# Kernel tuning notes

Measured on AMD Instinct MI355X. Metric: run time of the kernel, lower is better.

The kernel has to match this reference:

```python
import jax, jax.numpy as jnp
import numpy as np

N = 5000        # n_stocks (nodes)
F = 128         # n_features
H = 4           # attention heads
C = 32          # hidden_size per head
HC = H * C      # GAT output dim = GRU input dim
GH = 256        # gru_hidden_size
E = 320000      # directed edges (before self-loops)
NEG_SLOPE = 0.2 # GATv2Conv default leaky_relu slope


def setup_inputs() -> dict:
    key = jax.random.key(0)
    ks = jax.random.split(key, 16)
    s = 0.05
    return {
        "x": jax.random.normal(ks[0], (N, F), dtype=jnp.float32),
        "edge_index": jax.random.randint(ks[1], (2, E), 0, N, dtype=jnp.int64),
        # GATv2Conv params (lin_l, lin_r with bias, attention vector, output bias)
        "W_l": jax.random.normal(ks[2], (F, HC), dtype=jnp.float32) * s,
        "b_l": jax.random.normal(ks[3], (HC,), dtype=jnp.float32) * s,
        "W_r": jax.random.normal(ks[4], (F, HC), dtype=jnp.float32) * s,
        "b_r": jax.random.normal(ks[5], (HC,), dtype=jnp.float32) * s,
        "att": jax.random.normal(ks[6], (H, C), dtype=jnp.float32) * s,
        "gat_bias": jax.random.normal(ks[7], (HC,), dtype=jnp.float32) * s,
        # GRU params (single layer, PyTorch gate order r,z,n)
        "W_ih": jax.random.normal(ks[8], (3 * GH, HC), dtype=jnp.float32) * s,
        "W_hh": jax.random.normal(ks[9], (3 * GH, GH), dtype=jnp.float32) * s,
        "b_ih": jax.random.normal(ks[10], (3 * GH,), dtype=jnp.float32) * s,
        "b_hh": jax.random.normal(ks[11], (3 * GH,), dtype=jnp.float32) * s,
        # policy head + log_std param
        "Wp": jax.random.normal(ks[12], (N, GH), dtype=jnp.float32) * s,
        "bp": jax.random.normal(ks[13], (N,), dtype=jnp.float32) * s,
        "log_std": jnp.zeros((N,), dtype=jnp.float32),
    }


def reference(x, edge_index, W_l, b_l, W_r, b_r, att, gat_bias,
              W_ih, W_hh, b_ih, b_hh, Wp, bp, log_std):
    # --- GATv2Conv (add_self_loops=True, concat heads, eval mode -> no dropout) ---
    loop = jnp.arange(N, dtype=edge_index.dtype)
    src = jnp.concatenate([edge_index[0], loop])  # message source j
    dst = jnp.concatenate([edge_index[1], loop])  # message target i

    xl = (x @ W_l + b_l).reshape(N, H, C)  # source-side transform
    xr = (x @ W_r + b_r).reshape(N, H, C)  # target-side transform

    m = xl[src] + xr[dst]                                  # [Etot, H, C]
    e = jnp.einsum('ehc,hc->eh', jax.nn.leaky_relu(m, NEG_SLOPE), att)

    # segment softmax over incoming edges per target node
    emax = jax.ops.segment_max(e, dst, num_segments=N)      # [N, H]
    ex = jnp.exp(e - emax[dst])
    denom = jax.ops.segment_sum(ex, dst, num_segments=N)    # [N, H]
    alpha = ex / denom[dst]                                 # [Etot, H]

    agg = jax.ops.segment_sum(alpha[:, :, None] * xl[src], dst, num_segments=N)
    gat_out = agg.reshape(N, HC) + gat_bias                 # [N, H*C]

    # --- GRU: each node = one batch element, seq_len=1, h0 = 0 ---
    gi = gat_out @ W_ih.T + b_ih                            # [N, 3*GH]
    gr, gz, gn = jnp.split(gi, 3, axis=1)
    hr, hz, hn = jnp.split(b_hh, 3)                          # h0=0 -> only hh bias
    r = jax.nn.sigmoid(gr + hr)
    z = jax.nn.sigmoid(gz + hz)
    n = jnp.tanh(gn + r * hn)
    h = (1.0 - z) * n                                        # [N, GH]

    # --- policy head ---
    mean = h @ Wp.T + bp                                     # [N, N]
    std = jnp.exp(jnp.clip(log_std, -10.0, 2.0))             # [N]
    return mean, std
```

## Files before the change

### kernel.cpp

```cpp
#include <hip/hip_runtime.h>
#include <hip/hip_bf16.h>
#include <float.h>

#define N_NODES 5000
#define F_IN    128
#define HC      128
#define GH      256
#define NE      320000
#define NET     325000
#define MPAD    5120
#define CAP     160
#define LIN_BLKS   313
#define DEC_BLKS  1270
#define NTHR    (DEC_BLKS * 256)

typedef __bf16 bf16;
typedef __attribute__((ext_vector_type(4))) __bf16 bf16x4;
typedef __attribute__((ext_vector_type(8))) __bf16 bf16x8;
typedef __attribute__((ext_vector_type(4))) float  f32x4;

__device__ __forceinline__ float lrelu(float v) { return v > 0.f ? v : 0.2f * v; }
__device__ __forceinline__ float sigm(float v) { return 1.f / (1.f + __expf(-v)); }

__device__ __forceinline__ void gload16(const void* g, void* l) {
  __builtin_amdgcn_global_load_lds((const __attribute__((address_space(1))) void*)g,
                                   (__attribute__((address_space(3))) void*)l, 16, 0, 0);
}

__global__ void k_init(int* __restrict__ cnt) {
  int i = blockIdx.x * 256 + threadIdx.x;
  if (i < N_NODES) cnt[i] = 0;
}

#define NWIH (768 * HC)
#define NWP  (N_NODES * GH)
__global__ __launch_bounds__(256) void k_pre(
    const float* __restrict__ x,
    const float* __restrict__ Wl, const float* __restrict__ bl,
    const float* __restrict__ Wr, const float* __restrict__ br,
    bf16* __restrict__ xlb, bf16* __restrict__ xrb,
    const float* __restrict__ lstd, float* __restrict__ out_std,
    const int* __restrict__ ei, int* __restrict__ cnt, int* __restrict__ csr_s,
    const float* __restrict__ wih, const float* __restrict__ wp,
    bf16* __restrict__ wihb, bf16* __restrict__ wpb) {
  __shared__ float xs[16][F_IN];
  int t = threadIdx.x;
  if (blockIdx.x < LIN_BLKS) {
    int nb = blockIdx.x * 16;
#pragma unroll
    for (int p = 0; p < 8; ++p) {
      int idx = p * 256 + t;
      int nl = idx >> 7, c = idx & 127;
      int gn = nb + nl;
      xs[nl][c] = (gn < N_NODES) ? x[(size_t)gn * F_IN + c] : 0.f;
    }
    __syncthreads();
    int col = t & 127;
    const float* W = (t < 128) ? Wl : Wr;
    float bias = (t < 128) ? bl[col] : br[col];
    float acc[16];
#pragma unroll
    for (int m = 0; m < 16; ++m) acc[m] = bias;
#pragma unroll 4
    for (int k = 0; k < F_IN; ++k) {
      float w = W[k * HC + col];
#pragma unroll
      for (int m = 0; m < 16; ++m) acc[m] = fmaf(xs[m][k], w, acc[m]);
    }
    bf16* out = (t < 128) ? xlb : xrb;
#pragma unroll
    for (int m = 0; m < 16; ++m) {
      int gn = nb + m;
      if (gn < N_NODES) out[(size_t)gn * HC + col] = (bf16)acc[m];
    }
    if (t < 16) {
      int gn = nb + t;
      if (gn < N_NODES) out_std[gn] = expf(fminf(fmaxf(lstd[gn], -10.f), 2.f));
    }
    return;
  }
  __shared__ int mode;
  if (t == 0) {
    int f = 0;
    for (int q = 1; q < 128; q += 2) f |= ei[q];
    mode = (f == 0) ? 1 : 0;
  }
  __syncthreads();
  int e = (blockIdx.x - LIN_BLKS) * 256 + t;
  for (int i = e; i < NWIH / 4; i += NTHR) {
    float4 v = reinterpret_cast<const float4*>(wih)[i];
    bf16x4 o = {(bf16)v.x, (bf16)v.y, (bf16)v.z, (bf16)v.w};
    *reinterpret_cast<bf16x4*>(&wihb[i * 4]) = o;
  }
  for (int i = e; i < NWP / 4; i += NTHR) {
    float4 v = reinterpret_cast<const float4*>(wp)[i];
    bf16x4 o = {(bf16)v.x, (bf16)v.y, (bf16)v.z, (bf16)v.w};
    *reinterpret_cast<bf16x4*>(&wpb[i * 4]) = o;
  }
  if (e >= NET) return;
  int s, d;
  if (e >= NE) { s = d = e - NE; }
  else if (mode) {
    int2 sv = *reinterpret_cast<const int2*>(&ei[2 * e]);
    int2 dv = *reinterpret_cast<const int2*>(&ei[2 * (NE + e)]);
    s = sv.x; d = dv.x;
  } else { s = ei[e]; d = ei[NE + e]; }
  int slot = atomicAdd(&cnt[d], 1);
  if (slot < CAP) csr_s[d * CAP + slot] = s;
}

__global__ __launch_bounds__(256) void k_gat(
    const bf16* __restrict__ xlb, const bf16* __restrict__ xrb,
    const int* __restrict__ csr_s, const int* __restrict__ cnt,
    const float* __restrict__ att, const float* __restrict__ gbias,
    bf16* __restrict__ gat_b) {
  int t = threadIdx.x;
  int lane = t & 63;
  int node = blockIdx.x * 4 + (t >> 6);
  if (node >= N_NODES) return;
  int c8 = lane & 15;
  int eg = lane >> 4;
  bf16x8 xr8 = *reinterpret_cast<const bf16x8*>(xrb + (size_t)node * HC + c8 * 8);
  float4 w0 = reinterpret_cast<const float4*>(att)[c8 * 2];
  float4 w1 = reinterpret_cast<const float4*>(att)[c8 * 2 + 1];
  float xr[8], wv[8];
#pragma unroll
  for (int k = 0; k < 8; ++k) xr[k] = (float)xr8[k];
  wv[0] = w0.x; wv[1] = w0.y; wv[2] = w0.z; wv[3] = w0.w;
  wv[4] = w1.x; wv[5] = w1.y; wv[6] = w1.z; wv[7] = w1.w;

  float acc[8] = {0.f, 0.f, 0.f, 0.f, 0.f, 0.f, 0.f, 0.f};
  float den = 0.f;
  int deg = cnt[node];
  deg = deg < CAP ? deg : CAP;
  int beg = node * CAP, end = node * CAP + deg;
#pragma unroll 2
  for (int p0 = beg; p0 < end; p0 += 4) {
    int p = p0 + eg;
    bool valid = p < end;
    int j = valid ? csr_s[p] : node;
    bf16x8 a8 = *reinterpret_cast<const bf16x8*>(xlb + (size_t)j * HC + c8 * 8);
    float av[8];
    float tt = 0.f;
#pragma unroll
    for (int k = 0; k < 8; ++k) {
      av[k] = (float)a8[k];
      tt = fmaf(lrelu(av[k] + xr[k]), wv[k], tt);
    }
    tt += __shfl_xor(tt, 1);
    tt += __shfl_xor(tt, 2);
    float pe = valid ? __expf(tt) : 0.f;
    den += pe;
#pragma unroll
    for (int k = 0; k < 8; ++k) acc[k] = fmaf(pe, av[k], acc[k]);
  }
#pragma unroll
  for (int m = 16; m <= 32; m <<= 1) {
    den += __shfl_xor(den, m);
#pragma unroll
    for (int k = 0; k < 8; ++k) acc[k] += __shfl_xor(acc[k], m);
  }
  if (eg == 0) {
    float4 g0 = reinterpret_cast<const float4*>(gbias)[c8 * 2];
    float4 g1 = reinterpret_cast<const float4*>(gbias)[c8 * 2 + 1];
    float gb[8] = {g0.x, g0.y, g0.z, g0.w, g1.x, g1.y, g1.z, g1.w};
    float rden = 1.f / den;
    bf16x8 o;
#pragma unroll
    for (int k = 0; k < 8; ++k) o[k] = (bf16)(acc[k] * rden + gb[k]);
    *reinterpret_cast<bf16x8*>(gat_b + (size_t)node * HC + c8 * 8) = o;
  }
}

__global__ __launch_bounds__(256) void k_gemm_gru(
    const bf16* __restrict__ A, const bf16* __restrict__ wihb,
    const float* __restrict__ bih, const float* __restrict__ bhh,
    bf16* __restrict__ hb) {
  __shared__ char smem[73728];
  char* Ab = smem;
  int t = threadIdx.x;
  int lane = t & 63, wave = t >> 6;
  int wm = wave >> 1, wn = wave & 1;
  int r16 = lane & 15, kg = lane >> 4;
  int sw7 = r16 & 7;
  int bm = blockIdx.x >> 1, bn = blockIdx.x & 1;
  int r0 = bm * 32, c0 = bn * 128;

#pragma unroll
  for (int q = 0; q < 2; ++q) {
    int idx = q * 256 + t;
    int half = idx >> 8, ih = idx & 255;
    int row = ih >> 3, cc = ih & 7;
    int gc = cc ^ (row & 7);
    gload16(&A[(size_t)(r0 + row) * 128 + half * 64 + gc * 8],
            Ab + (q * 256 + wave * 64) * 16);
  }

  auto STAGE_B = [&](int gate, int buf) {
    char* Bb = smem + 8192 + buf * 32768;
#pragma unroll
    for (int q = 0; q < 8; ++q) {
      int idx = q * 256 + t;
      int half = idx >> 10, ih = idx & 1023;
      int row = ih >> 3, cc = ih & 7;
      int gc = cc ^ (row & 7);
      gload16(&wihb[(size_t)(gate * 256 + c0 + row) * 128 + half * 64 + gc * 8],
              Bb + (q * 256 + wave * 64) * 16);
    }
  };

  int rowA = (wm * 16 + r16) * 128;
  int rowB[4];
#pragma unroll
  for (int n = 0; n < 4; ++n) rowB[n] = (wn * 64 + n * 16 + r16) * 128;

  f32x4 acc[3][4] = {};
  STAGE_B(0, 0);
  __syncthreads();
#pragma unroll
  for (int g = 0; g < 3; ++g) {
    if (g < 2) STAGE_B(g + 1, (g + 1) & 1);
    const char* Bb = smem + 8192 + (g & 1) * 32768;
#pragma unroll
    for (int h = 0; h < 2; ++h)
#pragma unroll
      for (int w = 0; w < 2; ++w) {
        int ch = ((w * 4 + kg) ^ sw7) * 16;
        bf16x8 af = *reinterpret_cast<const bf16x8*>(Ab + h * 4096 + rowA + ch);
        bf16x8 bfr[4];
#pragma unroll
        for (int n = 0; n < 4; ++n)
          bfr[n] = *reinterpret_cast<const bf16x8*>(Bb + h * 16384 + rowB[n] + ch);
#pragma unroll
        for (int n = 0; n < 4; ++n)
          acc[g][n] = __builtin_amdgcn_mfma_f32_16x16x32_bf16(af, bfr[n], acc[g][n], 0, 0, 0);
      }
    __syncthreads();
  }

  bf16* hl = (bf16*)Ab;
#pragma unroll
  for (int n = 0; n < 4; ++n) {
    int c = c0 + wn * 64 + n * 16 + r16;
    float bihr = bih[c],       bhhr = bhh[c];
    float bihz = bih[256 + c], bhhz = bhh[256 + c];
    float bihn = bih[512 + c], bhhn = bhh[512 + c];
#pragma unroll
    for (int rr = 0; rr < 4; ++rr) {
      float rg = sigm(acc[0][n][rr] + bihr + bhhr);
      float zg = sigm(acc[1][n][rr] + bihz + bhhz);
      float ng = tanhf(acc[2][n][rr] + bihn + rg * bhhn);
      float hv = (1.f - zg) * ng;
      int row = wm * 16 + kg * 4 + rr;
      hl[row * 128 + (wn * 64 + n * 16 + r16)] = (bf16)hv;
    }
  }
  __syncthreads();
#pragma unroll
  for (int q = 0; q < 2; ++q) {
    int idx = q * 256 + t;
    int row = idx >> 4, cc = idx & 15;
    *reinterpret_cast<int4*>(&hb[(size_t)(r0 + row) * GH + c0 + cc * 8]) =
        *reinterpret_cast<const int4*>(&hl[row * 128 + cc * 8]);
  }
}

__global__ __launch_bounds__(256) void gemm_nt_f32out(
    const bf16* __restrict__ A, const bf16* __restrict__ B,
    const float* __restrict__ bias, float* __restrict__ Cout,
    int K, int ldc, int Mstore, int Nstore, int nbx) {
  __shared__ char smem[65536];
  int t = threadIdx.x;
  int lane = t & 63, wave = t >> 6;
  int wm = wave >> 1, wn = wave & 1;
  int r16 = lane & 15, kg = lane >> 4;

  int nwg = gridDim.x;
  int cpx = nwg >> 3;
  int wg  = blockIdx.x;
  int swz = (wg & 7) * cpx + (wg >> 3);
  int bm0 = (swz % nbx) * 128;
  int bn0 = (swz / nbx) * 128;

  int rsub = lane >> 3;
  int cchk = lane & 7;

  auto STAGE = [&](int buf, int k0) {
    char* Ab = smem + buf * 32768;
#pragma unroll
    for (int q = 0; q < 4; ++q) {
      int row = (wave * 4 + q) * 8 + rsub;
      int gc = cchk ^ (row & 7);
      char* db = Ab + (wave * 4 + q) * 1024;
      gload16(&A[(size_t)(bm0 + row) * K + k0 + gc * 8], db);
      gload16(&B[(size_t)(bn0 + row) * K + k0 + gc * 8], db + 16384);
    }
  };

  f32x4 acc[4][4] = {};
  int rbA[4], rbB[4];
#pragma unroll
  for (int m = 0; m < 4; ++m) rbA[m] = (wm * 64 + m * 16 + r16) * 128;
#pragma unroll
  for (int n = 0; n < 4; ++n) rbB[n] = (wn * 64 + n * 16 + r16) * 128;
  int sw7 = r16 & 7;

  int nt = K >> 6;
  STAGE(0, 0);
  __syncthreads();
  for (int tt = 0; tt < nt; ++tt) {
    if (tt + 1 < nt) STAGE((tt & 1) ^ 1, (tt + 1) * 64);
    const char* Ab = smem + (tt & 1) * 32768;
    const char* Bb = Ab + 16384;
#pragma unroll
    for (int ks = 0; ks < 2; ++ks) {
      int ch = ((ks * 4 + kg) ^ sw7) * 16;
      bf16x8 af[4], bfr[4];
#pragma unroll
      for (int m = 0; m < 4; ++m)
        af[m] = *reinterpret_cast<const bf16x8*>(Ab + rbA[m] + ch);
#pragma unroll
      for (int n = 0; n < 4; ++n)
        bfr[n] = *reinterpret_cast<const bf16x8*>(Bb + rbB[n] + ch);
#pragma unroll
      for (int m = 0; m < 4; ++m)
#pragma unroll
        for (int n = 0; n < 4; ++n)
          acc[m][n] = __builtin_amdgcn_mfma_f32_16x16x32_bf16(af[m], bfr[n], acc[m][n], 0, 0, 0);
    }
    __syncthreads();
  }

  float bv[4];
#pragma unroll
  for (int n = 0; n < 4; ++n) {
    int gcol = bn0 + wn * 64 + n * 16 + r16;
    bv[n] = (gcol < Nstore) ? bias[gcol] : 0.f;
  }

  float* Cs = (float*)smem;
#pragma unroll
  for (int m = 0; m < 4; ++m) {
    int rb = wm * 64 + m * 16 + kg * 4;
#pragma unroll
    for (int n = 0; n < 4; ++n) {
      int cb = wn * 64 + n * 16 + r16;
#pragma unroll
      for (int r = 0; r < 4; ++r)
        Cs[(rb + r) * 128 + cb] = acc[m][n][r] + bv[n];
    }
  }
  __syncthreads();
#pragma unroll
  for (int i = 0; i < 16; ++i) {
    int chunk = i * 256 + t;
    int row = chunk >> 5, cc = chunk & 31;
    int grow = bm0 + row, gcol = bn0 + cc * 4;
    if (grow < Mstore && gcol < Nstore) {
      f32x4 v = *reinterpret_cast<const f32x4*>(&Cs[row * 128 + cc * 4]);
      __builtin_nontemporal_store(v, reinterpret_cast<f32x4*>(&Cout[(size_t)grow * ldc + gcol]));
    }
  }
}

extern "C" void kernel_launch(void* const* d_in, const int* in_sizes, int n_in,
                              void* d_out, int out_size, void* d_ws, size_t ws_size,
                              hipStream_t stream) {
  const float* x     = (const float*)d_in[0];
  const int*   ei    = (const int*)d_in[1];
  const float* Wl    = (const float*)d_in[2];
  const float* bl    = (const float*)d_in[3];
  const float* Wr    = (const float*)d_in[4];
  const float* br    = (const float*)d_in[5];
  const float* att   = (const float*)d_in[6];
  const float* gbias = (const float*)d_in[7];
  const float* Wih   = (const float*)d_in[8];
  const float* bih   = (const float*)d_in[10];
  const float* bhh   = (const float*)d_in[11];
  const float* Wp    = (const float*)d_in[12];
  const float* bp    = (const float*)d_in[13];
  const float* lstd  = (const float*)d_in[14];
  float* out_mean = (float*)d_out;
  float* out_std  = out_mean + (size_t)N_NODES * N_NODES;

  char* w = (char*)d_ws;
  auto carve = [&](size_t bytes) {
    char* p = w; w += (bytes + 255) & ~(size_t)255; return p;
  };
  bf16*  xlb   = (bf16*)carve((size_t)N_NODES * HC * 2);
  bf16*  xrb   = (bf16*)carve((size_t)N_NODES * HC * 2);
  int*   cnt   = (int*)carve((size_t)N_NODES * 4);
  int*   csr_s = (int*)carve((size_t)N_NODES * CAP * 4);
  bf16*  gatb  = (bf16*)carve((size_t)MPAD * HC * 2);
  bf16*  wihb  = (bf16*)carve((size_t)768 * HC * 2);
  bf16*  hb    = (bf16*)carve((size_t)MPAD * GH * 2);
  bf16*  wpb   = (bf16*)carve((size_t)MPAD * GH * 2);

  k_init<<<(N_NODES + 255) / 256, 256, 0, stream>>>(cnt);
  k_pre<<<LIN_BLKS + DEC_BLKS, 256, 0, stream>>>(
      x, Wl, bl, Wr, br, xlb, xrb, lstd, out_std,
      ei, cnt, csr_s, Wih, Wp, wihb, wpb);
  k_gat<<<(N_NODES + 3) / 4, 256, 0, stream>>>(xlb, xrb, csr_s, cnt, att, gbias, gatb);
  k_gemm_gru<<<320, 256, 0, stream>>>(gatb, wihb, bih, bhh, hb);
  gemm_nt_f32out<<<40 * 40, 256, 0, stream>>>(hb, wpb, bp, out_mean, 256, N_NODES, N_NODES, N_NODES, 40);
}
```

Before: 110.6 us.

## Load GEMM A fragments directly from global and halve LDS footprint

Measured after the change: 125.2 us. 1.13x slower.

```diff
diff --git a/kernel.cpp b/kernel.cpp
--- a/kernel.cpp
+++ b/kernel.cpp
@@ -269,11 +269,12 @@
     const bf16* __restrict__ A, const bf16* __restrict__ B,
     const float* __restrict__ bias, float* __restrict__ Cout,
     int K, int ldc, int Mstore, int Nstore, int nbx) {
-  __shared__ char smem[65536];
+  __shared__ char smem[32768];
   int t = threadIdx.x;
   int lane = t & 63, wave = t >> 6;
   int wm = wave >> 1, wn = wave & 1;
   int r16 = lane & 15, kg = lane >> 4;
+  int sw7 = r16 & 7;
 
   int nwg = gridDim.x;
   int cpx = nwg >> 3;
@@ -285,40 +286,40 @@
   int rsub = lane >> 3;
   int cchk = lane & 7;
 
-  auto STAGE = [&](int buf, int k0) {
-    char* Ab = smem + buf * 32768;
+  auto STAGE_B = [&](int buf, int k0) {
+    char* Bb = smem + buf * 16384;
 #pragma unroll
     for (int q = 0; q < 4; ++q) {
       int row = (wave * 4 + q) * 8 + rsub;
       int gc = cchk ^ (row & 7);
-      char* db = Ab + (wave * 4 + q) * 1024;
-      gload16(&A[(size_t)(bm0 + row) * K + k0 + gc * 8], db);
-      gload16(&B[(size_t)(bn0 + row) * K + k0 + gc * 8], db + 16384);
+      gload16(&B[(size_t)(bn0 + row) * K + k0 + gc * 8], Bb + (wave * 4 + q) * 1024);
     }
   };
 
   f32x4 acc[4][4] = {};
-  int rbA[4], rbB[4];
-#pragma unroll
-  for (int m = 0; m < 4; ++m) rbA[m] = (wm * 64 + m * 16 + r16) * 128;
+  int rbB[4];
 #pragma unroll
   for (int n = 0; n < 4; ++n) rbB[n] = (wn * 64 + n * 16 + r16) * 128;
-  int sw7 = r16 & 7;
+  const bf16* Arow[4];
+#pragma unroll
+  for (int m = 0; m < 4; ++m)
+    Arow[m] = A + (size_t)(bm0 + wm * 64 + m * 16 + r16) * K;
 
   int nt = K >> 6;
-  STAGE(0, 0);
+  STAGE_B(0, 0);
   __syncthreads();
   for (int tt = 0; tt < nt; ++tt) {
-    if (tt + 1 < nt) STAGE((tt & 1) ^ 1, (tt + 1) * 64);
-    const char* Ab = smem + (tt & 1) * 32768;
-    const char* Bb = Ab + 16384;
+    if (tt + 1 < nt) STAGE_B((tt & 1) ^ 1, (tt + 1) * 64);
+    const char* Bb = smem + (tt & 1) * 16384;
+    int k0 = tt * 64;
 #pragma unroll
     for (int ks = 0; ks < 2; ++ks) {
       int ch = ((ks * 4 + kg) ^ sw7) * 16;
+      int ka = k0 + ks * 32 + kg * 8;
       bf16x8 af[4], bfr[4];
 #pragma unroll
       for (int m = 0; m < 4; ++m)
-        af[m] = *reinterpret_cast<const bf16x8*>(Ab + rbA[m] + ch);
+        af[m] = *reinterpret_cast<const bf16x8*>(Arow[m] + ka);
 #pragma unroll
       for (int n = 0; n < 4; ++n)
         bfr[n] = *reinterpret_cast<const bf16x8*>(Bb + rbB[n] + ch);
@@ -339,27 +340,32 @@
   }
 
   float* Cs = (float*)smem;
-#pragma unroll
-  for (int m = 0; m < 4; ++m) {
-    int rb = wm * 64 + m * 16 + kg * 4;
-#pragma unroll
-    for (int n = 0; n < 4; ++n) {
-      int cb = wn * 64 + n * 16 + r16;
-#pragma unroll
-      for (int r = 0; r < 4; ++r)
-        Cs[(rb + r) * 128 + cb] = acc[m][n][r] + bv[n];
-    }
-  }
-  __syncthreads();
-#pragma unroll
-  for (int i = 0; i < 16; ++i) {
-    int chunk = i * 256 + t;
-    int row = chunk >> 5, cc = chunk & 31;
-    int grow = bm0 + row, gcol = bn0 + cc * 4;
-    if (grow < Mstore && gcol < Nstore) {
-      f32x4 v = *reinterpret_cast<const f32x4*>(&Cs[row * 128 + cc * 4]);
-      __builtin_nontemporal_store(v, reinterpret_cast<f32x4*>(&Cout[(size_t)grow * ldc + gcol]));
-    }
+  for (int h = 0; h < 2; ++h) {
+    if (wm == h) {
+#pragma unroll
+      for (int m = 0; m < 4; ++m) {
+        int rb = m * 16 + kg * 4;
+#pragma unroll
+        for (int n = 0; n < 4; ++n) {
+          int cb = wn * 64 + n * 16 + r16;
+#pragma unroll
+          for (int r = 0; r < 4; ++r)
+            Cs[(rb + r) * 128 + cb] = acc[m][n][r] + bv[n];
+        }
+      }
+    }
+    __syncthreads();
+#pragma unroll
+    for (int i = 0; i < 8; ++i) {
+      int chunk = i * 256 + t;
+      int row = chunk >> 5, cc = chunk & 31;
+      int grow = bm0 + h * 64 + row, gcol = bn0 + cc * 4;
+      if (grow < Mstore && gcol < Nstore) {
+        f32x4 v = *reinterpret_cast<const f32x4*>(&Cs[row * 128 + cc * 4]);
+        __builtin_nontemporal_store(v, reinterpret_cast<f32x4*>(&Cout[(size_t)grow * ldc + gcol]));
+      }
+    }
+    __syncthreads();
   }
 }
 
```
